# Kernel optimization log

Hardware: AMD Instinct MI355X
Metric: run time of the kernel (lower is better)

Reference implementation:

```python
import jax, jax.numpy as jnp
import numpy as np

B, NW = 1024, 300
N = NW // 3          # 100 tokens (keypoints)
E = 5                # token dim after cat of PE(2): 3 + 2
H, D, L = 4, 64, 3   # heads, d_attention, layers


def setup_inputs() -> dict:
    key = jax.random.key(0)
    ks = jax.random.split(key, 8)
    s = jnp.float32(0.1)
    x = jax.random.normal(ks[0], (B, NW), dtype=jnp.float32)
    Wq = jax.random.normal(ks[1], (L, H, D, E), dtype=jnp.float32) * s  # per-head W_Q (no bias)
    Wk = jax.random.normal(ks[2], (L, H, D, E), dtype=jnp.float32) * s
    Wv = jax.random.normal(ks[3], (L, H, D, E), dtype=jnp.float32) * s
    Wo = jax.random.normal(ks[4], (L, E, H * D), dtype=jnp.float32) * s  # MHA output proj (no bias)
    Wf = jax.random.normal(ks[5], (L, E, E), dtype=jnp.float32) * s      # FFN linear
    bf = jax.random.normal(ks[6], (L, E), dtype=jnp.float32) * s
    g1 = jnp.ones((L, E), dtype=jnp.float32)
    b1 = jnp.zeros((L, E), dtype=jnp.float32)
    g2 = jnp.ones((L, E), dtype=jnp.float32)
    b2 = jnp.zeros((L, E), dtype=jnp.float32)
    return dict(x=x, Wq=Wq, Wk=Wk, Wv=Wv, Wo=Wo, Wf=Wf, bf=bf,
                g1=g1, b1=b1, g2=g2, b2=b2)


def _layer_norm(x, g, b, eps=1e-5):
    mu = jnp.mean(x, axis=-1, keepdims=True)
    var = jnp.mean((x - mu) ** 2, axis=-1, keepdims=True)  # biased, like torch LN
    return (x - mu) / jnp.sqrt(var + eps) * g + b


def reference(x, Wq, Wk, Wv, Wo, Wf, bf, g1, b1, g2, b2):
    kp = x.reshape(B, N, 3)                      # 'b (n d) -> b n d', d=3
    mask = kp[:, :, -1] > 0                      # [B,N] keypoint confidence mask
    # PositionalEncoding(d_model=2, kind='cat'): div_term=[1] -> pe=[sin(pos),cos(pos)]
    pos = jnp.arange(N, dtype=jnp.float32)
    pe = jnp.stack([jnp.sin(pos), jnp.cos(pos)], axis=-1)         # [N,2]
    out = jnp.concatenate([kp, jnp.broadcast_to(pe, (B, N, 2))], axis=-1)  # [B,N,5]
    out = jnp.where(mask[:, :, None], out, jnp.float32(0.0))      # out[~mask]=0

    pair = mask[:, None, None, :] & mask[:, None, :, None]        # [B,1,N,N]
    neg = -jnp.finfo(jnp.float32).max
    scale = jnp.float32(1.0 / np.sqrt(D))
    for l in range(L):
        # per-head projections (heads vectorized over h)
        q = jnp.einsum('bne,hde->bhnd', out, Wq[l])
        k = jnp.einsum('bne,hde->bhnd', out, Wk[l])
        v = jnp.einsum('bne,hde->bhnd', out, Wv[l])
        dots = jnp.einsum('bhid,bhjd->bhij', q, k) * scale        # [B,H,N,N]
        dots = jnp.where(pair, dots, neg)
        attn = jax.nn.softmax(dots, axis=-1)
        o = jnp.einsum('bhij,bhjd->bhid', attn, v)                # [B,H,N,D]
        o = o.transpose(0, 2, 1, 3).reshape(B, N, H * D)          # concat heads
        attn_out = o @ Wo[l].T                                    # [B,N,E]
        ln1 = _layer_norm(attn_out + out, g1[l], b1[l])
        ffn = jax.nn.relu(ln1 @ Wf[l].T + bf[l])
        out = _layer_norm(ffn + ln1, g2[l], b2[l])
    return out
```

## Files before the change

### kernel.cpp

```cpp
#include <hip/hip_runtime.h>
#include <math.h>

#define NTOK 100
#define EDIM 5
#define NH   4
#define NL   3
#define DD   64
#define BLK  256

__global__ void precompute_mp(const float* __restrict__ Wq,
                              const float* __restrict__ Wk,
                              const float* __restrict__ Wv,
                              const float* __restrict__ Wo,
                              float* __restrict__ mp) {
  const int blk = blockIdx.x;
  const int which = blk / 12;
  const int rem = blk % 12;
  const int l = rem / 4, h = rem % 4;
  const int t = threadIdx.x;

  __shared__ float A[320];
  __shared__ float Bsh[320];

  const float* wa = (which ? Wv : Wq) + (l*NH + h)*DD*EDIM;
  for (int r = t; r < 320; r += 64) A[r] = wa[r];
  if (which == 0) {
    const float* wk = Wk + (l*NH + h)*DD*EDIM;
    for (int r = t; r < 320; r += 64) Bsh[r] = wk[r];
  } else {
    for (int r = t; r < 320; r += 64) {
      int f = r >> 6, d = r & 63;
      Bsh[r] = Wo[(l*EDIM + f)*(NH*DD) + h*DD + d];
    }
  }
  __syncthreads();
  if (t < 25) {
    int e = t / 5, f = t % 5;
    float acc = 0.f;
    if (which == 0) {
      #pragma unroll 8
      for (int d = 0; d < DD; ++d) acc += A[d*5+e] * Bsh[d*5+f];
      acc *= 0.125f;
    } else {
      #pragma unroll 8
      for (int d = 0; d < DD; ++d) acc += A[d*5+e] * Bsh[f*64+d];
    }
    mp[which*960 + ((l*NH + h)*EDIM + e)*8 + f] = acc;
  }
}

__global__ __launch_bounds__(BLK) void encoder_kernel(
    const float* __restrict__ x,
    const float* __restrict__ mp,
    const float* __restrict__ Wf,
    const float* __restrict__ bfv,
    const float* __restrict__ g1,
    const float* __restrict__ b1,
    const float* __restrict__ g2,
    const float* __restrict__ b2,
    float* __restrict__ out)
{
  const int b = blockIdx.x, t = threadIdx.x;

  __shared__ float4 s_MP4[480];
  __shared__ float4 s_o4[NTOK+2];
  __shared__ float  s_o1[NTOK+2];
  __shared__ float4 s_w4[2][NH][NTOK+2];
  __shared__ float2 s_w2[2][NH][NTOK+2];
  __shared__ int    s_cidx[NTOK];
  __shared__ unsigned long long s_bal[2];

  const float* mpf = (const float*)s_MP4;

  for (int r = t; r < 480; r += BLK) s_MP4[r] = ((const float4*)mp)[r];

  float k0=0.f, k1=0.f, k2=0.f, msk=0.f;
  if (t < NTOK) {
    k0 = x[b*300 + 3*t];
    k1 = x[b*300 + 3*t + 1];
    k2 = x[b*300 + 3*t + 2];
    msk = (k2 > 0.f) ? 1.f : 0.f;
  }
  unsigned long long bal = __ballot(t < NTOK && msk != 0.f);
  if (t == 0)  s_bal[0] = bal;
  if (t == 64) s_bal[1] = bal;
  __syncthreads();
  const unsigned long long bw0 = s_bal[0], bw1 = s_bal[1];
  const int nm = __popcll(bw0) + __popcll(bw1);
  if (t < NTOK) {
    int lane = t & 63;
    unsigned long long lm = (lane == 0) ? 0ull : ((1ull << lane) - 1ull);
    int pre = (t < 64) ? __popcll(bw0 & lm) : (__popcll(bw0) + __popcll(bw1 & lm));
    if (msk != 0.f) {
      s_o4[pre] = make_float4(k0, k1, k2, sinf((float)t));
      s_o1[pre] = cosf((float)t);
      s_cidx[t] = pre;
    } else {
      s_cidx[t] = nm;
    }
  }
  if (t == 0) {
    s_o4[nm]   = make_float4(0.f,0.f,0.f,0.f); s_o1[nm]   = 0.f;
    s_o4[nm+1] = make_float4(0.f,0.f,0.f,0.f); s_o1[nm+1] = 0.f;
  }
  __syncthreads();

  const int hp   = (nm + 2) >> 1;
  const int natt = NH * hp;
  const int nsplit = (2*natt <= BLK) ? 2 : 1;
  const bool task = (t < natt*nsplit);
  int h = 0, i0 = 0, i1 = 0, i1r = 0, jlo = 0, jhi = 0;
  bool rep0 = false, rep1 = false, w1ok = false;
  if (task) {
    int g  = t / natt;
    int tt = t - g*natt;
    h = tt / hp; i0 = tt - h*hp; i1 = i0 + hp;
    i1r = (i1 <= nm) ? i1 : nm;
    w1ok = (i1 <= nm);
    rep0 = (i0 == nm); rep1 = (i1 == nm);
    int jmid = nm >> 1;
    if (nsplit == 2) { jlo = g ? jmid : 0; jhi = g ? nm : jmid; }
    else             { jlo = 0; jhi = nm; }
  }
  const int wg = task ? (t / natt) : 0;

  for (int l = 0; l < NL; ++l) {
    if (task) {
      const float* Mh = mpf + ((l*NH + h)*EDIM)*8;
      float4 oA = s_o4[i0];  float oA4 = s_o1[i0];
      float4 oB = s_o4[i1r]; float oB4 = s_o1[i1r];
      float oa[5] = {oA.x, oA.y, oA.z, oA.w, oA4};
      float ob[5] = {oB.x, oB.y, oB.z, oB.w, oB4};
      float a0[5], a1[5];
      #pragma unroll
      for (int f = 0; f < 5; ++f) { a0[f] = 0.f; a1[f] = 0.f; }
      #pragma unroll
      for (int e = 0; e < 5; ++e) {
        float4 mr = *(const float4*)(Mh + e*8); float m4 = Mh[e*8+4];
        float va = oa[e], vb = ob[e];
        a0[0] += va*mr.x; a0[1] += va*mr.y; a0[2] += va*mr.z; a0[3] += va*mr.w; a0[4] += va*m4;
        a1[0] += vb*mr.x; a1[1] += vb*mr.y; a1[2] += vb*mr.z; a1[3] += vb*mr.w; a1[4] += vb*m4;
      }

      float ls0=0.f, ls1=0.f;
      float w00=0.f,w01=0.f,w02=0.f,w03=0.f,w04=0.f;
      float w10=0.f,w11=0.f,w12=0.f,w13=0.f,w14=0.f;
      #pragma unroll 4
      for (int j = jlo; j < jhi; ++j) {
        float4 oj = s_o4[j]; float oe = s_o1[j];
        float s0 = a0[0]*oj.x + a0[1]*oj.y + a0[2]*oj.z + a0[3]*oj.w + a0[4]*oe;
        float s1 = a1[0]*oj.x + a1[1]*oj.y + a1[2]*oj.z + a1[3]*oj.w + a1[4]*oe;
        float p0 = rep0 ? 1.f : __expf(s0);
        float p1 = rep1 ? 1.f : __expf(s1);
        ls0 += p0; ls1 += p1;
        w00 += p0*oj.x; w01 += p0*oj.y; w02 += p0*oj.z; w03 += p0*oj.w; w04 += p0*oe;
        w10 += p1*oj.x; w11 += p1*oj.y; w12 += p1*oj.z; w13 += p1*oj.w; w14 += p1*oe;
      }
      s_w4[wg][h][i0] = make_float4(w00, w01, w02, w03);
      s_w2[wg][h][i0] = make_float2(w04, ls0);
      if (w1ok) {
        s_w4[wg][h][i1] = make_float4(w10, w11, w12, w13);
        s_w2[wg][h][i1] = make_float2(w14, ls1);
      }
    }
    __syncthreads();

    if (t <= nm) {
      int i = t;
      bool rep = (i == nm);
      float4 ov = s_o4[i]; float ov4 = s_o1[i];
      float o[5] = {ov.x, ov.y, ov.z, ov.w, ov4};
      float wext = rep ? (float)(NTOK - nm) : 0.f;
      float c[5] = {0.f, 0.f, 0.f, 0.f, 0.f};
      #pragma unroll
      for (int hh = 0; hh < NH; ++hh) {
        float4 wa = s_w4[0][hh][i]; float2 wb = s_w2[0][hh][i];
        float w[5] = {wa.x, wa.y, wa.z, wa.w, wb.x};
        float ls = wb.y;
        if (nsplit == 2) {
          float4 wa2 = s_w4[1][hh][i]; float2 wb2 = s_w2[1][hh][i];
          w[0] += wa2.x; w[1] += wa2.y; w[2] += wa2.z; w[3] += wa2.w; w[4] += wb2.x;
          ls += wb2.y;
        }
        #pragma unroll
        for (int e = 0; e < 5; ++e) w[e] += wext * o[e];
        float inv = 1.f / (rep ? (float)NTOK : ls);
        const float* Ph = mpf + 960 + ((l*NH + hh)*EDIM)*8;
        #pragma unroll
        for (int e = 0; e < 5; ++e) {
          float4 pr = *(const float4*)(Ph + e*8); float p4 = Ph[e*8+4];
          float we = w[e] * inv;
          c[0] += we*pr.x; c[1] += we*pr.y; c[2] += we*pr.z; c[3] += we*pr.w; c[4] += we*p4;
        }
      }
      float y[5];
      #pragma unroll
      for (int e = 0; e < 5; ++e) y[e] = o[e] + c[e];
      float mu = 0.2f*(y[0]+y[1]+y[2]+y[3]+y[4]);
      float var = 0.f;
      #pragma unroll
      for (int e = 0; e < 5; ++e) { float d = y[e]-mu; var += d*d; }
      var *= 0.2f;
      float inv = 1.f / sqrtf(var + 1e-5f);
      float ln1[5];
      #pragma unroll
      for (int e = 0; e < 5; ++e) ln1[e] = (y[e]-mu)*inv*g1[l*5+e] + b1[l*5+e];
      float r2[5];
      #pragma unroll
      for (int e = 0; e < 5; ++e) {
        float acc = bfv[l*5+e];
        #pragma unroll
        for (int f = 0; f < 5; ++f) acc += ln1[f]*Wf[(l*5+e)*5+f];
        acc = acc > 0.f ? acc : 0.f;
        r2[e] = acc + ln1[e];
      }
      float mu2 = 0.2f*(r2[0]+r2[1]+r2[2]+r2[3]+r2[4]);
      float var2 = 0.f;
      #pragma unroll
      for (int e = 0; e < 5; ++e) { float d = r2[e]-mu2; var2 += d*d; }
      var2 *= 0.2f;
      float inv2 = 1.f / sqrtf(var2 + 1e-5f);
      float no0 = (r2[0]-mu2)*inv2*g2[l*5+0] + b2[l*5+0];
      float no1 = (r2[1]-mu2)*inv2*g2[l*5+1] + b2[l*5+1];
      float no2 = (r2[2]-mu2)*inv2*g2[l*5+2] + b2[l*5+2];
      float no3 = (r2[3]-mu2)*inv2*g2[l*5+3] + b2[l*5+3];
      float no4 = (r2[4]-mu2)*inv2*g2[l*5+4] + b2[l*5+4];
      s_o4[i] = make_float4(no0, no1, no2, no3);
      s_o1[i] = no4;
    }
    __syncthreads();
  }

  for (int r = t; r < NTOK*EDIM; r += BLK) {
    int i = r / EDIM;
    int e = r - i*EDIM;
    int c = s_cidx[i];
    float v = (e < 4) ? ((const float*)&s_o4[c])[e] : s_o1[c];
    out[b*(NTOK*EDIM) + r] = v;
  }
}

extern "C" void kernel_launch(void* const* d_in, const int* in_sizes, int n_in,
                              void* d_out, int out_size, void* d_ws, size_t ws_size,
                              hipStream_t stream) {
  const float* x  = (const float*)d_in[0];
  const float* Wq = (const float*)d_in[1];
  const float* Wk = (const float*)d_in[2];
  const float* Wv = (const float*)d_in[3];
  const float* Wo = (const float*)d_in[4];
  const float* Wf = (const float*)d_in[5];
  const float* bf = (const float*)d_in[6];
  const float* g1 = (const float*)d_in[7];
  const float* b1 = (const float*)d_in[8];
  const float* g2 = (const float*)d_in[9];
  const float* b2 = (const float*)d_in[10];
  float* outp = (float*)d_out;
  float* mp   = (float*)d_ws;

  precompute_mp<<<24, 64, 0, stream>>>(Wq, Wk, Wv, Wo, mp);
  encoder_kernel<<<1024, BLK, 0, stream>>>(x, mp, Wf, bf, g1, b1, g2, b2, outp);
}
```

Measured before the change: 120.9 us.

## Assign one wavefront per head with replicated token state and double-buffered partials

Restructures the attention work so each wavefront owns one head and each lane owns one query row. Every wavefront also keeps its own copy of the token state and redundantly computes the LayerNorm/FFN update, which removes one block barrier per layer by double-buffering the per-head output partials. Output projection is now applied per head before the cross-head reduction, and log2(e) is folded into the QK matrix so exp2f can replace __expf. It also raises launch bounds to request 4 blocks per CU. The cost is redundant FFN/LN work in all four waves, more shared memory, and a second pass when more than 63 tokens are masked in, since a lane then handles two rows serially over the full key loop.

```diff
diff --git a/kernel.cpp b/kernel.cpp
--- a/kernel.cpp
+++ b/kernel.cpp
@@ -40,7 +40,7 @@
     if (which == 0) {
       #pragma unroll 8
       for (int d = 0; d < DD; ++d) acc += A[d*5+e] * Bsh[d*5+f];
-      acc *= 0.125f;
+      acc *= 0.125f * 1.44269504088896340736f;
     } else {
       #pragma unroll 8
       for (int d = 0; d < DD; ++d) acc += A[d*5+e] * Bsh[f*64+d];
@@ -49,7 +49,7 @@
   }
 }
 
-__global__ __launch_bounds__(BLK) void encoder_kernel(
+__global__ __launch_bounds__(BLK, 4) void encoder_kernel(
     const float* __restrict__ x,
     const float* __restrict__ mp,
     const float* __restrict__ Wf,
@@ -61,17 +61,18 @@
     float* __restrict__ out)
 {
   const int b = blockIdx.x, t = threadIdx.x;
+  const int wv = t >> 6;
+  const int ln = t & 63;
 
   __shared__ float4 s_MP4[480];
-  __shared__ float4 s_o4[NTOK+2];
-  __shared__ float  s_o1[NTOK+2];
-  __shared__ float4 s_w4[2][NH][NTOK+2];
-  __shared__ float2 s_w2[2][NH][NTOK+2];
+  __shared__ float4 s_o4[NH][NTOK+2];
+  __shared__ float  s_o1[NH][NTOK+2];
+  __shared__ float4 s_wp4[2][NH][NTOK+2];
+  __shared__ float  s_wp1[2][NH][NTOK+2];
   __shared__ int    s_cidx[NTOK];
   __shared__ unsigned long long s_bal[2];
 
   const float* mpf = (const float*)s_MP4;
-
   for (int r = t; r < 480; r += BLK) s_MP4[r] = ((const float4*)mp)[r];
 
   float k0=0.f, k1=0.f, k2=0.f, msk=0.f;
@@ -92,150 +93,129 @@
     unsigned long long lm = (lane == 0) ? 0ull : ((1ull << lane) - 1ull);
     int pre = (t < 64) ? __popcll(bw0 & lm) : (__popcll(bw0) + __popcll(bw1 & lm));
     if (msk != 0.f) {
-      s_o4[pre] = make_float4(k0, k1, k2, sinf((float)t));
-      s_o1[pre] = cosf((float)t);
+      float4 v = make_float4(k0, k1, k2, sinf((float)t));
+      float v4 = cosf((float)t);
+      #pragma unroll
+      for (int w = 0; w < NH; ++w) { s_o4[w][pre] = v; s_o1[w][pre] = v4; }
       s_cidx[t] = pre;
     } else {
       s_cidx[t] = nm;
     }
   }
   if (t == 0) {
-    s_o4[nm]   = make_float4(0.f,0.f,0.f,0.f); s_o1[nm]   = 0.f;
-    s_o4[nm+1] = make_float4(0.f,0.f,0.f,0.f); s_o1[nm+1] = 0.f;
-  }
-  __syncthreads();
-
-  const int hp   = (nm + 2) >> 1;
-  const int natt = NH * hp;
-  const int nsplit = (2*natt <= BLK) ? 2 : 1;
-  const bool task = (t < natt*nsplit);
-  int h = 0, i0 = 0, i1 = 0, i1r = 0, jlo = 0, jhi = 0;
-  bool rep0 = false, rep1 = false, w1ok = false;
-  if (task) {
-    int g  = t / natt;
-    int tt = t - g*natt;
-    h = tt / hp; i0 = tt - h*hp; i1 = i0 + hp;
-    i1r = (i1 <= nm) ? i1 : nm;
-    w1ok = (i1 <= nm);
-    rep0 = (i0 == nm); rep1 = (i1 == nm);
-    int jmid = nm >> 1;
-    if (nsplit == 2) { jlo = g ? jmid : 0; jhi = g ? nm : jmid; }
-    else             { jlo = 0; jhi = nm; }
-  }
-  const int wg = task ? (t / natt) : 0;
+    #pragma unroll
+    for (int w = 0; w < NH; ++w) {
+      s_o4[w][nm] = make_float4(0.f,0.f,0.f,0.f);
+      s_o1[w][nm] = 0.f;
+    }
+  }
+  __syncthreads();
+
+  const int rows = nm + 1;
+  const int npass = (rows > 64) ? 2 : 1;
+  const float4* ow4 = s_o4[wv];
+  const float*  ow1 = s_o1[wv];
+  int bufp = 0;
 
   for (int l = 0; l < NL; ++l) {
-    if (task) {
-      const float* Mh = mpf + ((l*NH + h)*EDIM)*8;
-      float4 oA = s_o4[i0];  float oA4 = s_o1[i0];
-      float4 oB = s_o4[i1r]; float oB4 = s_o1[i1r];
-      float oa[5] = {oA.x, oA.y, oA.z, oA.w, oA4};
-      float ob[5] = {oB.x, oB.y, oB.z, oB.w, oB4};
-      float a0[5], a1[5];
-      #pragma unroll
-      for (int f = 0; f < 5; ++f) { a0[f] = 0.f; a1[f] = 0.f; }
-      #pragma unroll
-      for (int e = 0; e < 5; ++e) {
-        float4 mr = *(const float4*)(Mh + e*8); float m4 = Mh[e*8+4];
-        float va = oa[e], vb = ob[e];
-        a0[0] += va*mr.x; a0[1] += va*mr.y; a0[2] += va*mr.z; a0[3] += va*mr.w; a0[4] += va*m4;
-        a1[0] += vb*mr.x; a1[1] += vb*mr.y; a1[2] += vb*mr.z; a1[3] += vb*mr.w; a1[4] += vb*m4;
-      }
-
-      float ls0=0.f, ls1=0.f;
-      float w00=0.f,w01=0.f,w02=0.f,w03=0.f,w04=0.f;
-      float w10=0.f,w11=0.f,w12=0.f,w13=0.f,w14=0.f;
-      #pragma unroll 4
-      for (int j = jlo; j < jhi; ++j) {
-        float4 oj = s_o4[j]; float oe = s_o1[j];
-        float s0 = a0[0]*oj.x + a0[1]*oj.y + a0[2]*oj.z + a0[3]*oj.w + a0[4]*oe;
-        float s1 = a1[0]*oj.x + a1[1]*oj.y + a1[2]*oj.z + a1[3]*oj.w + a1[4]*oe;
-        float p0 = rep0 ? 1.f : __expf(s0);
-        float p1 = rep1 ? 1.f : __expf(s1);
-        ls0 += p0; ls1 += p1;
-        w00 += p0*oj.x; w01 += p0*oj.y; w02 += p0*oj.z; w03 += p0*oj.w; w04 += p0*oe;
-        w10 += p1*oj.x; w11 += p1*oj.y; w12 += p1*oj.z; w13 += p1*oj.w; w14 += p1*oe;
-      }
-      s_w4[wg][h][i0] = make_float4(w00, w01, w02, w03);
-      s_w2[wg][h][i0] = make_float2(w04, ls0);
-      if (w1ok) {
-        s_w4[wg][h][i1] = make_float4(w10, w11, w12, w13);
-        s_w2[wg][h][i1] = make_float2(w14, ls1);
-      }
-    }
-    __syncthreads();
-
-    if (t <= nm) {
-      int i = t;
-      bool rep = (i == nm);
-      float4 ov = s_o4[i]; float ov4 = s_o1[i];
-      float o[5] = {ov.x, ov.y, ov.z, ov.w, ov4};
-      float wext = rep ? (float)(NTOK - nm) : 0.f;
-      float c[5] = {0.f, 0.f, 0.f, 0.f, 0.f};
-      #pragma unroll
-      for (int hh = 0; hh < NH; ++hh) {
-        float4 wa = s_w4[0][hh][i]; float2 wb = s_w2[0][hh][i];
-        float w[5] = {wa.x, wa.y, wa.z, wa.w, wb.x};
-        float ls = wb.y;
-        if (nsplit == 2) {
-          float4 wa2 = s_w4[1][hh][i]; float2 wb2 = s_w2[1][hh][i];
-          w[0] += wa2.x; w[1] += wa2.y; w[2] += wa2.z; w[3] += wa2.w; w[4] += wb2.x;
-          ls += wb2.y;
-        }
-        #pragma unroll
-        for (int e = 0; e < 5; ++e) w[e] += wext * o[e];
+    const float* Mh = mpf + ((l*NH + wv)*EDIM)*8;
+    const float* Ph = mpf + 960 + ((l*NH + wv)*EDIM)*8;
+
+    for (int ps = 0; ps < npass; ++ps) {
+      const int i = ln + (ps << 6);
+      if (i < rows) {
+        const bool rep = (i == nm);
+        float4 ov = ow4[i]; float ov4 = ow1[i];
+        float o_[5] = {ov.x, ov.y, ov.z, ov.w, ov4};
+        float a0=0.f,a1=0.f,a2=0.f,a3=0.f,a4=0.f;
+        #pragma unroll
+        for (int e = 0; e < 5; ++e) {
+          float4 mr = *(const float4*)(Mh + e*8); float m4 = Mh[e*8+4];
+          a0 += o_[e]*mr.x; a1 += o_[e]*mr.y; a2 += o_[e]*mr.z;
+          a3 += o_[e]*mr.w; a4 += o_[e]*m4;
+        }
+        if (rep) { a0=0.f; a1=0.f; a2=0.f; a3=0.f; a4=0.f; }
+
+        float w0=0.f,w1=0.f,w2=0.f,w3=0.f,w4=0.f, ls=0.f;
+        #pragma unroll 4
+        for (int j = 0; j < nm; ++j) {
+          float4 oj = ow4[j]; float oe = ow1[j];
+          float s = a0*oj.x + a1*oj.y + a2*oj.z + a3*oj.w + a4*oe;
+          float p = exp2f(s);
+          ls += p;
+          w0 += p*oj.x; w1 += p*oj.y; w2 += p*oj.z; w3 += p*oj.w; w4 += p*oe;
+        }
+        if (rep) {
+          float wext = (float)(NTOK - nm);
+          w0 += wext*o_[0]; w1 += wext*o_[1]; w2 += wext*o_[2];
+          w3 += wext*o_[3]; w4 += wext*o_[4];
+        }
         float inv = 1.f / (rep ? (float)NTOK : ls);
-        const float* Ph = mpf + 960 + ((l*NH + hh)*EDIM)*8;
+        float we[5] = {w0,w1,w2,w3,w4};
+        float c0=0.f,c1=0.f,c2=0.f,c3=0.f,c4=0.f;
         #pragma unroll
         for (int e = 0; e < 5; ++e) {
           float4 pr = *(const float4*)(Ph + e*8); float p4 = Ph[e*8+4];
-          float we = w[e] * inv;
-          c[0] += we*pr.x; c[1] += we*pr.y; c[2] += we*pr.z; c[3] += we*pr.w; c[4] += we*p4;
-        }
+          c0 += we[e]*pr.x; c1 += we[e]*pr.y; c2 += we[e]*pr.z;
+          c3 += we[e]*pr.w; c4 += we[e]*p4;
+        }
+        s_wp4[bufp][wv][i] = make_float4(c0*inv, c1*inv, c2*inv, c3*inv);
+        s_wp1[bufp][wv][i] = c4*inv;
       }
-      float y[5];
-      #pragma unroll
-      for (int e = 0; e < 5; ++e) y[e] = o[e] + c[e];
-      float mu = 0.2f*(y[0]+y[1]+y[2]+y[3]+y[4]);
-      float var = 0.f;
-      #pragma unroll
-      for (int e = 0; e < 5; ++e) { float d = y[e]-mu; var += d*d; }
-      var *= 0.2f;
-      float inv = 1.f / sqrtf(var + 1e-5f);
-      float ln1[5];
-      #pragma unroll
-      for (int e = 0; e < 5; ++e) ln1[e] = (y[e]-mu)*inv*g1[l*5+e] + b1[l*5+e];
-      float r2[5];
-      #pragma unroll
-      for (int e = 0; e < 5; ++e) {
-        float acc = bfv[l*5+e];
-        #pragma unroll
-        for (int f = 0; f < 5; ++f) acc += ln1[f]*Wf[(l*5+e)*5+f];
-        acc = acc > 0.f ? acc : 0.f;
-        r2[e] = acc + ln1[e];
+    }
+    __syncthreads();
+
+    for (int ps = 0; ps < npass; ++ps) {
+      const int i = ln + (ps << 6);
+      if (i < rows) {
+        float4 ov = ow4[i]; float ov4 = ow1[i];
+        float y[5] = {ov.x, ov.y, ov.z, ov.w, ov4};
+        #pragma unroll
+        for (int hh = 0; hh < NH; ++hh) {
+          float4 wa = s_wp4[bufp][hh][i];
+          y[0] += wa.x; y[1] += wa.y; y[2] += wa.z; y[3] += wa.w;
+          y[4] += s_wp1[bufp][hh][i];
+        }
+        float mu = 0.2f*(y[0]+y[1]+y[2]+y[3]+y[4]);
+        float var = 0.f;
+        #pragma unroll
+        for (int e = 0; e < 5; ++e) { float d = y[e]-mu; var += d*d; }
+        var *= 0.2f;
+        float inv1 = 1.f / sqrtf(var + 1e-5f);
+        float ln1[5];
+        #pragma unroll
+        for (int e = 0; e < 5; ++e) ln1[e] = (y[e]-mu)*inv1*g1[l*5+e] + b1[l*5+e];
+        float r2[5];
+        #pragma unroll
+        for (int e = 0; e < 5; ++e) {
+          float acc = bfv[l*5+e];
+          #pragma unroll
+          for (int f = 0; f < 5; ++f) acc += ln1[f]*Wf[(l*5+e)*5+f];
+          acc = acc > 0.f ? acc : 0.f;
+          r2[e] = acc + ln1[e];
+        }
+        float mu2 = 0.2f*(r2[0]+r2[1]+r2[2]+r2[3]+r2[4]);
+        float var2 = 0.f;
+        #pragma unroll
+        for (int e = 0; e < 5; ++e) { float d = r2[e]-mu2; var2 += d*d; }
+        var2 *= 0.2f;
+        float inv2 = 1.f / sqrtf(var2 + 1e-5f);
+        float no[5];
+        #pragma unroll
+        for (int e = 0; e < 5; ++e) no[e] = (r2[e]-mu2)*inv2*g2[l*5+e] + b2[l*5+e];
+        s_o4[wv][i] = make_float4(no[0], no[1], no[2], no[3]);
+        s_o1[wv][i] = no[4];
       }
-      float mu2 = 0.2f*(r2[0]+r2[1]+r2[2]+r2[3]+r2[4]);
-      float var2 = 0.f;
-      #pragma unroll
-      for (int e = 0; e < 5; ++e) { float d = r2[e]-mu2; var2 += d*d; }
-      var2 *= 0.2f;
-      float inv2 = 1.f / sqrtf(var2 + 1e-5f);
-      float no0 = (r2[0]-mu2)*inv2*g2[l*5+0] + b2[l*5+0];
-      float no1 = (r2[1]-mu2)*inv2*g2[l*5+1] + b2[l*5+1];
-      float no2 = (r2[2]-mu2)*inv2*g2[l*5+2] + b2[l*5+2];
-      float no3 = (r2[3]-mu2)*inv2*g2[l*5+3] + b2[l*5+3];
-      float no4 = (r2[4]-mu2)*inv2*g2[l*5+4] + b2[l*5+4];
-      s_o4[i] = make_float4(no0, no1, no2, no3);
-      s_o1[i] = no4;
-    }
-    __syncthreads();
-  }
+    }
+    bufp ^= 1;
+  }
+  __syncthreads();
 
   for (int r = t; r < NTOK*EDIM; r += BLK) {
     int i = r / EDIM;
     int e = r - i*EDIM;
     int c = s_cidx[i];
-    float v = (e < 4) ? ((const float*)&s_o4[c])[e] : s_o1[c];
+    float v = (e < 4) ? ((const float*)&s_o4[0][c])[e] : s_o1[0][c];
     out[b*(NTOK*EDIM) + r] = v;
   }
 }
```

Result: slower. 138.9 us (+14.9%).

## Fold log2e into QK matrix, move output projection into attention threads, use fast intrinsics

Applied to the files above, without the earlier changes.

Scales the precomputed QK bilinear matrix by log2(e) so the score loop can use a raw v_exp_f32 (exp2) through inline asm. For the padding-representative row it zeroes the score coefficients instead of branching per element. The per-head output projection now runs inside the attention threads before the partial sums go to shared memory, so the combine stage only adds up pre-projected partials scaled by a reciprocal. LayerNorm and FFN constants are staged in shared memory, and rcp/rsq/sin/cos use hardware approximations with launch_bounds occupancy 4. This trades some precision for fewer instructions in the serial per-token stage.

```diff
diff --git a/kernel.cpp b/kernel.cpp
--- a/kernel.cpp
+++ b/kernel.cpp
@@ -7,6 +7,10 @@
 #define NL   3
 #define DD   64
 #define BLK  256
+
+__device__ __forceinline__ float fexp2(float x){ float r; asm("v_exp_f32 %0, %1" : "=v"(r) : "v"(x)); return r; }
+__device__ __forceinline__ float frcp (float x){ float r; asm("v_rcp_f32 %0, %1" : "=v"(r) : "v"(x)); return r; }
+__device__ __forceinline__ float frsq (float x){ float r; asm("v_rsq_f32 %0, %1" : "=v"(r) : "v"(x)); return r; }
 
 __global__ void precompute_mp(const float* __restrict__ Wq,
                               const float* __restrict__ Wk,
@@ -40,7 +44,7 @@
     if (which == 0) {
       #pragma unroll 8
       for (int d = 0; d < DD; ++d) acc += A[d*5+e] * Bsh[d*5+f];
-      acc *= 0.125f;
+      acc *= 0.125f * 1.44269504088896340736f;
     } else {
       #pragma unroll 8
       for (int d = 0; d < DD; ++d) acc += A[d*5+e] * Bsh[f*64+d];
@@ -49,7 +53,7 @@
   }
 }
 
-__global__ __launch_bounds__(BLK) void encoder_kernel(
+__global__ __launch_bounds__(BLK, 4) void encoder_kernel(
     const float* __restrict__ x,
     const float* __restrict__ mp,
     const float* __restrict__ Wf,
@@ -67,12 +71,23 @@
   __shared__ float  s_o1[NTOK+2];
   __shared__ float4 s_w4[2][NH][NTOK+2];
   __shared__ float2 s_w2[2][NH][NTOK+2];
+  __shared__ float  s_cf[152];
   __shared__ int    s_cidx[NTOK];
   __shared__ unsigned long long s_bal[2];
 
   const float* mpf = (const float*)s_MP4;
 
   for (int r = t; r < 480; r += BLK) s_MP4[r] = ((const float4*)mp)[r];
+  for (int r = t; r < 150; r += BLK) {
+    float v;
+    if      (r <  75) v = Wf[r];
+    else if (r <  90) v = bfv[r-75];
+    else if (r < 105) v = g1[r-90];
+    else if (r < 120) v = b1[r-105];
+    else if (r < 135) v = g2[r-120];
+    else              v = b2[r-135];
+    s_cf[r] = v;
+  }
 
   float k0=0.f, k1=0.f, k2=0.f, msk=0.f;
   if (t < NTOK) {
@@ -86,14 +101,14 @@
   if (t == 64) s_bal[1] = bal;
   __syncthreads();
   const unsigned long long bw0 = s_bal[0], bw1 = s_bal[1];
-  const int nm = __popcll(bw0) + __popcll(bw1);
+  const int nm = __builtin_amdgcn_readfirstlane(__popcll(bw0) + __popcll(bw1));
   if (t < NTOK) {
     int lane = t & 63;
     unsigned long long lm = (lane == 0) ? 0ull : ((1ull << lane) - 1ull);
     int pre = (t < 64) ? __popcll(bw0 & lm) : (__popcll(bw0) + __popcll(bw1 & lm));
     if (msk != 0.f) {
-      s_o4[pre] = make_float4(k0, k1, k2, sinf((float)t));
-      s_o1[pre] = cosf((float)t);
+      s_o4[pre] = make_float4(k0, k1, k2, __sinf((float)t));
+      s_o1[pre] = __cosf((float)t);
       s_cidx[t] = pre;
     } else {
       s_cidx[t] = nm;
@@ -110,7 +125,7 @@
   const int nsplit = (2*natt <= BLK) ? 2 : 1;
   const bool task = (t < natt*nsplit);
   int h = 0, i0 = 0, i1 = 0, i1r = 0, jlo = 0, jhi = 0;
-  bool rep0 = false, rep1 = false, w1ok = false;
+  bool rep0 = false, rep1 = false, w1ok = false, corr = false;
   if (task) {
     int g  = t / natt;
     int tt = t - g*natt;
@@ -118,11 +133,13 @@
     i1r = (i1 <= nm) ? i1 : nm;
     w1ok = (i1 <= nm);
     rep0 = (i0 == nm); rep1 = (i1 == nm);
+    corr = (g == 0);
     int jmid = nm >> 1;
     if (nsplit == 2) { jlo = g ? jmid : 0; jhi = g ? nm : jmid; }
     else             { jlo = 0; jhi = nm; }
   }
   const int wg = task ? (t / natt) : 0;
+  const float wext = (float)(NTOK - nm);
 
   for (int l = 0; l < NL; ++l) {
     if (task) {
@@ -141,6 +158,8 @@
         a0[0] += va*mr.x; a0[1] += va*mr.y; a0[2] += va*mr.z; a0[3] += va*mr.w; a0[4] += va*m4;
         a1[0] += vb*mr.x; a1[1] += vb*mr.y; a1[2] += vb*mr.z; a1[3] += vb*mr.w; a1[4] += vb*m4;
       }
+      if (rep0) { a0[0]=0.f; a0[1]=0.f; a0[2]=0.f; a0[3]=0.f; a0[4]=0.f; }
+      if (rep1) { a1[0]=0.f; a1[1]=0.f; a1[2]=0.f; a1[3]=0.f; a1[4]=0.f; }
 
       float ls0=0.f, ls1=0.f;
       float w00=0.f,w01=0.f,w02=0.f,w03=0.f,w04=0.f;
@@ -148,19 +167,40 @@
       #pragma unroll 4
       for (int j = jlo; j < jhi; ++j) {
         float4 oj = s_o4[j]; float oe = s_o1[j];
-        float s0 = a0[0]*oj.x + a0[1]*oj.y + a0[2]*oj.z + a0[3]*oj.w + a0[4]*oe;
-        float s1 = a1[0]*oj.x + a1[1]*oj.y + a1[2]*oj.z + a1[3]*oj.w + a1[4]*oe;
-        float p0 = rep0 ? 1.f : __expf(s0);
-        float p1 = rep1 ? 1.f : __expf(s1);
+        float s0 = (a0[0]*oj.x + a0[1]*oj.y) + ((a0[2]*oj.z + a0[3]*oj.w) + a0[4]*oe);
+        float s1 = (a1[0]*oj.x + a1[1]*oj.y) + ((a1[2]*oj.z + a1[3]*oj.w) + a1[4]*oe);
+        float p0 = fexp2(s0);
+        float p1 = fexp2(s1);
         ls0 += p0; ls1 += p1;
         w00 += p0*oj.x; w01 += p0*oj.y; w02 += p0*oj.z; w03 += p0*oj.w; w04 += p0*oe;
         w10 += p1*oj.x; w11 += p1*oj.y; w12 += p1*oj.z; w13 += p1*oj.w; w14 += p1*oe;
       }
-      s_w4[wg][h][i0] = make_float4(w00, w01, w02, w03);
-      s_w2[wg][h][i0] = make_float2(w04, ls0);
+      if (rep0 && corr) {
+        w00 += wext*oa[0]; w01 += wext*oa[1]; w02 += wext*oa[2];
+        w03 += wext*oa[3]; w04 += wext*oa[4];
+      }
+      if (rep1 && corr) {
+        w10 += wext*ob[0]; w11 += wext*ob[1]; w12 += wext*ob[2];
+        w13 += wext*ob[3]; w14 += wext*ob[4];
+      }
+
+      const float* Ph = mpf + 960 + ((l*NH + h)*EDIM)*8;
+      float wr0[5] = {w00,w01,w02,w03,w04};
+      float wr1[5] = {w10,w11,w12,w13,w14};
+      float c00=0.f,c01=0.f,c02=0.f,c03=0.f,c04=0.f;
+      float c10=0.f,c11=0.f,c12=0.f,c13=0.f,c14=0.f;
+      #pragma unroll
+      for (int e = 0; e < 5; ++e) {
+        float4 pr = *(const float4*)(Ph + e*8); float p4 = Ph[e*8+4];
+        float va = wr0[e], vb = wr1[e];
+        c00 += va*pr.x; c01 += va*pr.y; c02 += va*pr.z; c03 += va*pr.w; c04 += va*p4;
+        c10 += vb*pr.x; c11 += vb*pr.y; c12 += vb*pr.z; c13 += vb*pr.w; c14 += vb*p4;
+      }
+      s_w4[wg][h][i0] = make_float4(c00, c01, c02, c03);
+      s_w2[wg][h][i0] = make_float2(c04, ls0);
       if (w1ok) {
-        s_w4[wg][h][i1] = make_float4(w10, w11, w12, w13);
-        s_w2[wg][h][i1] = make_float2(w14, ls1);
+        s_w4[wg][h][i1] = make_float4(c10, c11, c12, c13);
+        s_w2[wg][h][i1] = make_float2(c14, ls1);
       }
     }
     __syncthreads();
@@ -169,62 +209,48 @@
       int i = t;
       bool rep = (i == nm);
       float4 ov = s_o4[i]; float ov4 = s_o1[i];
-      float o[5] = {ov.x, ov.y, ov.z, ov.w, ov4};
-      float wext = rep ? (float)(NTOK - nm) : 0.f;
-      float c[5] = {0.f, 0.f, 0.f, 0.f, 0.f};
+      float y[5] = {ov.x, ov.y, ov.z, ov.w, ov4};
       #pragma unroll
       for (int hh = 0; hh < NH; ++hh) {
         float4 wa = s_w4[0][hh][i]; float2 wb = s_w2[0][hh][i];
-        float w[5] = {wa.x, wa.y, wa.z, wa.w, wb.x};
+        float c0 = wa.x, c1 = wa.y, c2 = wa.z, c3 = wa.w, c4 = wb.x;
         float ls = wb.y;
         if (nsplit == 2) {
           float4 wa2 = s_w4[1][hh][i]; float2 wb2 = s_w2[1][hh][i];
-          w[0] += wa2.x; w[1] += wa2.y; w[2] += wa2.z; w[3] += wa2.w; w[4] += wb2.x;
+          c0 += wa2.x; c1 += wa2.y; c2 += wa2.z; c3 += wa2.w; c4 += wb2.x;
           ls += wb2.y;
         }
-        #pragma unroll
-        for (int e = 0; e < 5; ++e) w[e] += wext * o[e];
-        float inv = 1.f / (rep ? (float)NTOK : ls);
-        const float* Ph = mpf + 960 + ((l*NH + hh)*EDIM)*8;
-        #pragma unroll
-        for (int e = 0; e < 5; ++e) {
-          float4 pr = *(const float4*)(Ph + e*8); float p4 = Ph[e*8+4];
-          float we = w[e] * inv;
-          c[0] += we*pr.x; c[1] += we*pr.y; c[2] += we*pr.z; c[3] += we*pr.w; c[4] += we*p4;
-        }
-      }
-      float y[5];
-      #pragma unroll
-      for (int e = 0; e < 5; ++e) y[e] = o[e] + c[e];
+        float inv = rep ? 0.01f : frcp(ls);
+        y[0] += c0*inv; y[1] += c1*inv; y[2] += c2*inv; y[3] += c3*inv; y[4] += c4*inv;
+      }
       float mu = 0.2f*(y[0]+y[1]+y[2]+y[3]+y[4]);
       float var = 0.f;
       #pragma unroll
       for (int e = 0; e < 5; ++e) { float d = y[e]-mu; var += d*d; }
-      var *= 0.2f;
-      float inv = 1.f / sqrtf(var + 1e-5f);
-      float ln1[5];
-      #pragma unroll
-      for (int e = 0; e < 5; ++e) ln1[e] = (y[e]-mu)*inv*g1[l*5+e] + b1[l*5+e];
+      float iv = frsq(var*0.2f + 1e-5f);
+      float l1[5];
+      #pragma unroll
+      for (int e = 0; e < 5; ++e)
+        l1[e] = (y[e]-mu)*iv*s_cf[90+l*5+e] + s_cf[105+l*5+e];
       float r2[5];
       #pragma unroll
       for (int e = 0; e < 5; ++e) {
-        float acc = bfv[l*5+e];
+        float acc = s_cf[75+l*5+e];
         #pragma unroll
-        for (int f = 0; f < 5; ++f) acc += ln1[f]*Wf[(l*5+e)*5+f];
+        for (int f = 0; f < 5; ++f) acc += l1[f]*s_cf[l*25+e*5+f];
         acc = acc > 0.f ? acc : 0.f;
-        r2[e] = acc + ln1[e];
+        r2[e] = acc + l1[e];
       }
       float mu2 = 0.2f*(r2[0]+r2[1]+r2[2]+r2[3]+r2[4]);
       float var2 = 0.f;
       #pragma unroll
       for (int e = 0; e < 5; ++e) { float d = r2[e]-mu2; var2 += d*d; }
-      var2 *= 0.2f;
-      float inv2 = 1.f / sqrtf(var2 + 1e-5f);
-      float no0 = (r2[0]-mu2)*inv2*g2[l*5+0] + b2[l*5+0];
-      float no1 = (r2[1]-mu2)*inv2*g2[l*5+1] + b2[l*5+1];
-      float no2 = (r2[2]-mu2)*inv2*g2[l*5+2] + b2[l*5+2];
-      float no3 = (r2[3]-mu2)*inv2*g2[l*5+3] + b2[l*5+3];
-      float no4 = (r2[4]-mu2)*inv2*g2[l*5+4] + b2[l*5+4];
+      float iv2 = frsq(var2*0.2f + 1e-5f);
+      float no0 = (r2[0]-mu2)*iv2*s_cf[120+l*5+0] + s_cf[135+l*5+0];
+      float no1 = (r2[1]-mu2)*iv2*s_cf[120+l*5+1] + s_cf[135+l*5+1];
+      float no2 = (r2[2]-mu2)*iv2*s_cf[120+l*5+2] + s_cf[135+l*5+2];
+      float no3 = (r2[3]-mu2)*iv2*s_cf[120+l*5+3] + s_cf[135+l*5+3];
+      float no4 = (r2[4]-mu2)*iv2*s_cf[120+l*5+4] + s_cf[135+l*5+4];
       s_o4[i] = make_float4(no0, no1, no2, no3);
       s_o1[i] = no4;
     }
```

After: 116.6 us. -3.6%, faster.
